# Kernel optimization log

Measured on AMD Instinct MI355X. Metric: run time of the kernel, lower is better.

Reference implementation:

```python
import jax, jax.numpy as jnp
import numpy as np


def setup_inputs() -> dict:
    key = jax.random.key(0)
    ks = jax.random.split(key, 7)
    B, V, D, H = 4, 1024, 3, 128
    vertices = jax.random.normal(ks[0], (B, V, D), dtype=jnp.float32)
    # Linear params (x @ W + b convention, W = torch_weight.T)
    W1 = jax.random.normal(ks[1], (2 * D, H), dtype=jnp.float32) * 0.05
    b1 = jnp.zeros((H,), dtype=jnp.float32)
    W2 = jax.random.normal(ks[2], (H, H // 2), dtype=jnp.float32) * 0.05
    b2 = jnp.zeros((H // 2,), dtype=jnp.float32)
    W3 = jax.random.normal(ks[3], (H // 2, 1), dtype=jnp.float32) * 0.05
    b3 = jnp.zeros((1,), dtype=jnp.float32)
    return {"vertices": vertices, "W1": W1, "b1": b1, "W2": W2, "b2": b2, "W3": W3, "b3": b3}


def reference(vertices, W1, b1, W2, b2, W3, b3):
    B, V, D = vertices.shape
    # All unordered pairs (i, j) with i < j -- same order as the nested loop.
    idx_i, idx_j = jnp.triu_indices(V, k=1)  # each [E], E = V*(V-1)/2
    # Pairwise edge features [B, E, 2D] via gather (no Python loop).
    edge_features = jnp.concatenate(
        [vertices[:, idx_i, :], vertices[:, idx_j, :]], axis=-1
    )
    # 3-layer MLP (dropout is identity in eval mode).
    x = jax.nn.relu(edge_features @ W1 + b1)   # [B, E, H]
    x = jax.nn.relu(x @ W2 + b2)               # [B, E, H//2]
    x = x @ W3 + b3                            # [B, E, 1]
    edge_probs = jax.nn.sigmoid(x[..., 0])     # [B, E]
    edge_indices = jnp.stack([idx_i, idx_j], axis=1)  # [E, 2]
    return edge_probs, edge_indices
```

## Files before the change

### kernel.cpp

```cpp
#include <hip/hip_runtime.h>
#include <hip/hip_bf16.h>
#include <math.h>

#define BB 4
#define VV 1024
#define HH 128
#define H2 64
#define EE 523776
#define BE (BB * EE)
#define TPB (EE / 16)
#define NTILES (BE / 16)
#define NTHR 256
#define NBLK 1024
#define NWAVE (NBLK * 4)

typedef __attribute__((ext_vector_type(8))) short bf16x8;
typedef __attribute__((ext_vector_type(4))) float f32x4;
typedef __attribute__((ext_vector_type(4))) unsigned u32x4;

__device__ __forceinline__ short f2bf(float f) {
    __hip_bfloat16 h = __float2bfloat16(f);
    return *reinterpret_cast<short*>(&h);
}

__device__ __forceinline__ unsigned pkbf(float lo, float hi) {
    return __builtin_amdgcn_perm(__float_as_uint(hi), __float_as_uint(lo),
                                 0x07060302u);
}

__device__ __forceinline__ bf16x8 relu_pack(f32x4 a, f32x4 b) {
    u32x4 r;
    r[0] = pkbf(fmaxf(a[0], 0.f), fmaxf(a[1], 0.f));
    r[1] = pkbf(fmaxf(a[2], 0.f), fmaxf(a[3], 0.f));
    r[2] = pkbf(fmaxf(b[0], 0.f), fmaxf(b[1], 0.f));
    r[3] = pkbf(fmaxf(b[2], 0.f), fmaxf(b[3], 0.f));
    return __builtin_bit_cast(bf16x8, r);
}

__global__ __launch_bounds__(NTHR, 3) void edge_mlp_v11(
    const float* __restrict__ vertices,
    const float* __restrict__ W1,
    const float* __restrict__ b1,
    const float* __restrict__ W2,
    const float* __restrict__ b2,
    const float* __restrict__ W3,
    const float* __restrict__ b3,
    float* __restrict__ out)
{
    __shared__ __align__(16) bf16x8 wA[10 * 64];
    __shared__ __align__(16) f32x4  wC[4 * 64];

    const int lane = threadIdx.x & 63;
    const int col  = lane & 15;
    const int u    = lane >> 4;
    const int wid  = threadIdx.x >> 6;

    const f32x4 zero4 = {0.f, 0.f, 0.f, 0.f};

    bf16x8 A2r[16];
#pragma unroll
    for (int mt = 0; mt < 4; ++mt) {
        const int n2 = 32 * (mt >> 1) + 8 * (col >> 2) + 4 * (mt & 1) + (col & 3);
#pragma unroll
        for (int p = 0; p < 4; ++p)
#pragma unroll
            for (int r = 0; r < 8; ++r)
                A2r[mt * 4 + p][r] = f2bf(W2[(32 * p + 8 * u + r) * H2 + n2]);
    }

    for (int f = wid; f < 14; f += 4) {
        if (f < 8) {
            const int p = f >> 1, q1 = f & 1;
            const int h = 32 * p + 8 * (col >> 2) + 4 * q1 + (col & 3);
            bf16x8 a;
#pragma unroll
            for (int r = 0; r < 8; ++r) {
                const int k = 8 * u + r;
                float w = 0.0f;
                if (k < 6)       w = W1[k * HH + h];
                else if (k == 6) w = b1[h];
                a[r] = f2bf(w);
            }
            wA[f * 64 + lane] = a;
        } else if (f < 10) {
            const int t = f - 8;
            bf16x8 a;
#pragma unroll
            for (int r = 0; r < 8; ++r) a[r] = f2bf(W3[32 * t + 8 * u + r]);
            wA[f * 64 + lane] = a;
        } else {
            const int mt = f - 10;
            f32x4 c;
#pragma unroll
            for (int q = 0; q < 4; ++q)
                c[q] = b2[32 * (mt >> 1) + 8 * u + 4 * (mt & 1) + q];
            wC[mt * 64 + lane] = c;
        }
    }
    const float b3v = b3[0];
    __syncthreads();

    const int gw = blockIdx.x * 4 + wid;

    for (int tt = gw; tt < NTILES; tt += NWAVE) {
        const int b  = tt / TPB;
        const int e0 = (tt - b * TPB) * 16;
        const int e  = e0 + col;

        const int rr = EE - 1 - e;
        const float sq = sqrtf((float)(8 * rr + 1));
        int m = (int)(0.5f * (sq - 1.0f));
        if ((m + 1) * (m + 2) / 2 <= rr) ++m;
        if (m * (m + 1) / 2 > rr) --m;
        const int pp = rr - m * (m + 1) / 2;
        const int iv = VV - 2 - m;
        const int jv = VV - 1 - pp;

        const float* pvi = vertices + (b * VV + iv) * 3;
        const float* pvj = vertices + (b * VV + jv) * 3;
        u32x4 fb;
        fb[0] = pkbf(pvi[0], pvi[1]);
        fb[1] = pkbf(pvi[2], pvj[0]);
        fb[2] = pkbf(pvj[1], pvj[2]);
        fb[3] = 0x00003F80u;
        const bf16x8 bfv = __builtin_bit_cast(bf16x8, fb);

        f32x4 d2_0 = wC[0 * 64 + lane];
        f32x4 d2_1 = wC[1 * 64 + lane];
        f32x4 d2_2 = wC[2 * 64 + lane];
        f32x4 d2_3 = wC[3 * 64 + lane];

#pragma unroll
        for (int p = 0; p < 4; ++p) {
            const bf16x8 a1a = wA[(2 * p + 0) * 64 + lane];
            const bf16x8 a1b = wA[(2 * p + 1) * 64 + lane];
            const f32x4 dA = __builtin_amdgcn_mfma_f32_16x16x32_bf16(a1a, bfv, zero4, 0, 0, 0);
            const f32x4 dB = __builtin_amdgcn_mfma_f32_16x16x32_bf16(a1b, bfv, zero4, 0, 0, 0);
            const bf16x8 Bh = relu_pack(dA, dB);
            d2_0 = __builtin_amdgcn_mfma_f32_16x16x32_bf16(A2r[0 * 4 + p], Bh, d2_0, 0, 0, 0);
            d2_1 = __builtin_amdgcn_mfma_f32_16x16x32_bf16(A2r[1 * 4 + p], Bh, d2_1, 0, 0, 0);
            d2_2 = __builtin_amdgcn_mfma_f32_16x16x32_bf16(A2r[2 * 4 + p], Bh, d2_2, 0, 0, 0);
            d2_3 = __builtin_amdgcn_mfma_f32_16x16x32_bf16(A2r[3 * 4 + p], Bh, d2_3, 0, 0, 0);
        }

        const bf16x8 Bh3_0 = relu_pack(d2_0, d2_1);
        const bf16x8 Bh3_1 = relu_pack(d2_2, d2_3);
        const bf16x8 a30 = wA[8 * 64 + lane];
        const bf16x8 a31 = wA[9 * 64 + lane];
        f32x4 d3 = {b3v, b3v, b3v, b3v};
        d3 = __builtin_amdgcn_mfma_f32_16x16x32_bf16(a30, Bh3_0, d3, 0, 0, 0);
        d3 = __builtin_amdgcn_mfma_f32_16x16x32_bf16(a31, Bh3_1, d3, 0, 0, 0);

        if (u == 0) {
            const float prob = __builtin_amdgcn_rcpf(1.0f + __expf(-d3[0]));
            out[tt * 16 + col] = prob;
            if (b == 0)
                *(float2*)(&out[BE + 2 * e]) = make_float2((float)iv, (float)jv);
        }
    }
}

extern "C" void kernel_launch(void* const* d_in, const int* in_sizes, int n_in,
                              void* d_out, int out_size, void* d_ws, size_t ws_size,
                              hipStream_t stream) {
    const float* vertices = (const float*)d_in[0];
    const float* W1 = (const float*)d_in[1];
    const float* b1 = (const float*)d_in[2];
    const float* W2 = (const float*)d_in[3];
    const float* b2 = (const float*)d_in[4];
    const float* W3 = (const float*)d_in[5];
    const float* b3 = (const float*)d_in[6];
    float* out = (float*)d_out;

    edge_mlp_v11<<<NBLK, NTHR, 0, stream>>>(vertices, W1, b1, W2, b2, W3, b3, out);
}
```

Before: 136.5 us.

## Process four 16-edge subtiles per wave iteration with W2 fragments in LDS

```diff
diff --git a/kernel.cpp b/kernel.cpp
--- a/kernel.cpp
+++ b/kernel.cpp
@@ -8,8 +8,8 @@
 #define H2 64
 #define EE 523776
 #define BE (BB * EE)
-#define TPB (EE / 16)
-#define NTILES (BE / 16)
+#define TPB64 (EE / 64)
+#define NT64 (BE / 64)
 #define NTHR 256
 #define NBLK 1024
 #define NWAVE (NBLK * 4)
@@ -37,7 +37,7 @@
     return __builtin_bit_cast(bf16x8, r);
 }
 
-__global__ __launch_bounds__(NTHR, 3) void edge_mlp_v11(
+__global__ __launch_bounds__(NTHR, 3) void edge_mlp_v12(
     const float* __restrict__ vertices,
     const float* __restrict__ W1,
     const float* __restrict__ b1,
@@ -47,7 +47,7 @@
     const float* __restrict__ b3,
     float* __restrict__ out)
 {
-    __shared__ __align__(16) bf16x8 wA[10 * 64];
+    __shared__ __align__(16) bf16x8 wA[26 * 64];
     __shared__ __align__(16) f32x4  wC[4 * 64];
 
     const int lane = threadIdx.x & 63;
@@ -57,18 +57,7 @@
 
     const f32x4 zero4 = {0.f, 0.f, 0.f, 0.f};
 
-    bf16x8 A2r[16];
-#pragma unroll
-    for (int mt = 0; mt < 4; ++mt) {
-        const int n2 = 32 * (mt >> 1) + 8 * (col >> 2) + 4 * (mt & 1) + (col & 3);
-#pragma unroll
-        for (int p = 0; p < 4; ++p)
-#pragma unroll
-            for (int r = 0; r < 8; ++r)
-                A2r[mt * 4 + p][r] = f2bf(W2[(32 * p + 8 * u + r) * H2 + n2]);
-    }
-
-    for (int f = wid; f < 14; f += 4) {
+    for (int f = wid; f < 30; f += 4) {
         if (f < 8) {
             const int p = f >> 1, q1 = f & 1;
             const int h = 32 * p + 8 * (col >> 2) + 4 * q1 + (col & 3);
@@ -82,14 +71,22 @@
                 a[r] = f2bf(w);
             }
             wA[f * 64 + lane] = a;
-        } else if (f < 10) {
-            const int t = f - 8;
+        } else if (f < 24) {
+            const int mt = (f - 8) >> 2, p = (f - 8) & 3;
+            const int n2 = 32 * (mt >> 1) + 8 * (col >> 2) + 4 * (mt & 1) + (col & 3);
+            bf16x8 a;
+#pragma unroll
+            for (int r = 0; r < 8; ++r)
+                a[r] = f2bf(W2[(32 * p + 8 * u + r) * H2 + n2]);
+            wA[f * 64 + lane] = a;
+        } else if (f < 26) {
+            const int t = f - 24;
             bf16x8 a;
 #pragma unroll
             for (int r = 0; r < 8; ++r) a[r] = f2bf(W3[32 * t + 8 * u + r]);
             wA[f * 64 + lane] = a;
         } else {
-            const int mt = f - 10;
+            const int mt = f - 26;
             f32x4 c;
 #pragma unroll
             for (int q = 0; q < 4; ++q)
@@ -102,60 +99,80 @@
 
     const int gw = blockIdx.x * 4 + wid;
 
-    for (int tt = gw; tt < NTILES; tt += NWAVE) {
-        const int b  = tt / TPB;
-        const int e0 = (tt - b * TPB) * 16;
-        const int e  = e0 + col;
+    for (int tt = gw; tt < NT64; tt += NWAVE) {
+        const int b  = tt / TPB64;
+        const int e0 = (tt - b * TPB64) * 64;
 
-        const int rr = EE - 1 - e;
-        const float sq = sqrtf((float)(8 * rr + 1));
-        int m = (int)(0.5f * (sq - 1.0f));
-        if ((m + 1) * (m + 2) / 2 <= rr) ++m;
-        if (m * (m + 1) / 2 > rr) --m;
-        const int pp = rr - m * (m + 1) / 2;
-        const int iv = VV - 2 - m;
-        const int jv = VV - 1 - pp;
+        bf16x8 bfv[4];
+        int iv[4], jv[4];
+#pragma unroll
+        for (int s = 0; s < 4; ++s) {
+            const int e  = e0 + s * 16 + col;
+            const int rr = EE - 1 - e;
+            const float sq = sqrtf((float)(8 * rr + 1));
+            int m = (int)(0.5f * (sq - 1.0f));
+            if ((m + 1) * (m + 2) / 2 <= rr) ++m;
+            if (m * (m + 1) / 2 > rr) --m;
+            const int pp = rr - m * (m + 1) / 2;
+            iv[s] = VV - 2 - m;
+            jv[s] = VV - 1 - pp;
+            const float* pvi = vertices + (b * VV + iv[s]) * 3;
+            const float* pvj = vertices + (b * VV + jv[s]) * 3;
+            u32x4 fb;
+            fb[0] = pkbf(pvi[0], pvi[1]);
+            fb[1] = pkbf(pvi[2], pvj[0]);
+            fb[2] = pkbf(pvj[1], pvj[2]);
+            fb[3] = 0x00003F80u;
+            bfv[s] = __builtin_bit_cast(bf16x8, fb);
+        }
 
-        const float* pvi = vertices + (b * VV + iv) * 3;
-        const float* pvj = vertices + (b * VV + jv) * 3;
-        u32x4 fb;
-        fb[0] = pkbf(pvi[0], pvi[1]);
-        fb[1] = pkbf(pvi[2], pvj[0]);
-        fb[2] = pkbf(pvj[1], pvj[2]);
-        fb[3] = 0x00003F80u;
-        const bf16x8 bfv = __builtin_bit_cast(bf16x8, fb);
-
-        f32x4 d2_0 = wC[0 * 64 + lane];
-        f32x4 d2_1 = wC[1 * 64 + lane];
-        f32x4 d2_2 = wC[2 * 64 + lane];
-        f32x4 d2_3 = wC[3 * 64 + lane];
+        f32x4 d2[4][4];
+#pragma unroll
+        for (int mt = 0; mt < 4; ++mt) {
+            const f32x4 c = wC[mt * 64 + lane];
+#pragma unroll
+            for (int s = 0; s < 4; ++s) d2[s][mt] = c;
+        }
 
 #pragma unroll
         for (int p = 0; p < 4; ++p) {
             const bf16x8 a1a = wA[(2 * p + 0) * 64 + lane];
             const bf16x8 a1b = wA[(2 * p + 1) * 64 + lane];
-            const f32x4 dA = __builtin_amdgcn_mfma_f32_16x16x32_bf16(a1a, bfv, zero4, 0, 0, 0);
-            const f32x4 dB = __builtin_amdgcn_mfma_f32_16x16x32_bf16(a1b, bfv, zero4, 0, 0, 0);
-            const bf16x8 Bh = relu_pack(dA, dB);
-            d2_0 = __builtin_amdgcn_mfma_f32_16x16x32_bf16(A2r[0 * 4 + p], Bh, d2_0, 0, 0, 0);
-            d2_1 = __builtin_amdgcn_mfma_f32_16x16x32_bf16(A2r[1 * 4 + p], Bh, d2_1, 0, 0, 0);
-            d2_2 = __builtin_amdgcn_mfma_f32_16x16x32_bf16(A2r[2 * 4 + p], Bh, d2_2, 0, 0, 0);
-            d2_3 = __builtin_amdgcn_mfma_f32_16x16x32_bf16(A2r[3 * 4 + p], Bh, d2_3, 0, 0, 0);
+            const bf16x8 w20 = wA[(8 + 0 * 4 + p) * 64 + lane];
+            const bf16x8 w21 = wA[(8 + 1 * 4 + p) * 64 + lane];
+            const bf16x8 w22 = wA[(8 + 2 * 4 + p) * 64 + lane];
+            const bf16x8 w23 = wA[(8 + 3 * 4 + p) * 64 + lane];
+#pragma unroll
+            for (int s = 0; s < 4; ++s) {
+                const f32x4 dA = __builtin_amdgcn_mfma_f32_16x16x32_bf16(a1a, bfv[s], zero4, 0, 0, 0);
+                const f32x4 dB = __builtin_amdgcn_mfma_f32_16x16x32_bf16(a1b, bfv[s], zero4, 0, 0, 0);
+                const bf16x8 Bh = relu_pack(dA, dB);
+                d2[s][0] = __builtin_amdgcn_mfma_f32_16x16x32_bf16(w20, Bh, d2[s][0], 0, 0, 0);
+                d2[s][1] = __builtin_amdgcn_mfma_f32_16x16x32_bf16(w21, Bh, d2[s][1], 0, 0, 0);
+                d2[s][2] = __builtin_amdgcn_mfma_f32_16x16x32_bf16(w22, Bh, d2[s][2], 0, 0, 0);
+                d2[s][3] = __builtin_amdgcn_mfma_f32_16x16x32_bf16(w23, Bh, d2[s][3], 0, 0, 0);
+            }
         }
 
-        const bf16x8 Bh3_0 = relu_pack(d2_0, d2_1);
-        const bf16x8 Bh3_1 = relu_pack(d2_2, d2_3);
-        const bf16x8 a30 = wA[8 * 64 + lane];
-        const bf16x8 a31 = wA[9 * 64 + lane];
-        f32x4 d3 = {b3v, b3v, b3v, b3v};
-        d3 = __builtin_amdgcn_mfma_f32_16x16x32_bf16(a30, Bh3_0, d3, 0, 0, 0);
-        d3 = __builtin_amdgcn_mfma_f32_16x16x32_bf16(a31, Bh3_1, d3, 0, 0, 0);
+        const bf16x8 a30 = wA[24 * 64 + lane];
+        const bf16x8 a31 = wA[25 * 64 + lane];
+#pragma unroll
+        for (int s = 0; s < 4; ++s) {
+            const bf16x8 Bh3_0 = relu_pack(d2[s][0], d2[s][1]);
+            const bf16x8 Bh3_1 = relu_pack(d2[s][2], d2[s][3]);
+            f32x4 d3 = {b3v, b3v, b3v, b3v};
+            d3 = __builtin_amdgcn_mfma_f32_16x16x32_bf16(a30, Bh3_0, d3, 0, 0, 0);
+            d3 = __builtin_amdgcn_mfma_f32_16x16x32_bf16(a31, Bh3_1, d3, 0, 0, 0);
 
-        if (u == 0) {
-            const float prob = __builtin_amdgcn_rcpf(1.0f + __expf(-d3[0]));
-            out[tt * 16 + col] = prob;
-            if (b == 0)
-                *(float2*)(&out[BE + 2 * e]) = make_float2((float)iv, (float)jv);
+            if (u == 0) {
+                const float prob = __builtin_amdgcn_rcpf(1.0f + __expf(-d3[0]));
+                out[tt * 64 + s * 16 + col] = prob;
+                if (b == 0) {
+                    const int e = e0 + s * 16 + col;
+                    *(float2*)(&out[BE + 2 * e]) =
+                        make_float2((float)iv[s], (float)jv[s]);
+                }
+            }
         }
     }
 }
@@ -172,5 +189,5 @@
     const float* b3 = (const float*)d_in[6];
     float* out = (float*)d_out;
 
-    edge_mlp_v11<<<NBLK, NTHR, 0, stream>>>(vertices, W1, b1, W2, b2, W3, b3, out);
+    edge_mlp_v12<<<NBLK, NTHR, 0, stream>>>(vertices, W1, b1, W2, b2, W3, b3, out);
 }
```

Measured after the change: 219.9 us. 61.0% more time.

## Precompute per-vertex layer-1 projections and replace layer-1 MFMAs with gathered adds

Applied to the files above, without the earlier changes.

```diff
diff --git a/kernel.cpp b/kernel.cpp
--- a/kernel.cpp
+++ b/kernel.cpp
@@ -13,6 +13,7 @@
 #define NTHR 256
 #define NBLK 1024
 #define NWAVE (NBLK * 4)
+#define PQN (BB * VV * HH)
 
 typedef __attribute__((ext_vector_type(8))) short bf16x8;
 typedef __attribute__((ext_vector_type(4))) float f32x4;
@@ -37,25 +38,37 @@
     return __builtin_bit_cast(bf16x8, r);
 }
 
-__global__ __launch_bounds__(NTHR, 3) void edge_mlp_v11(
-    const float* __restrict__ vertices,
-    const float* __restrict__ W1,
-    const float* __restrict__ b1,
+__global__ __launch_bounds__(NTHR) void pq_kernel(
+    const float* __restrict__ vertices, const float* __restrict__ W1,
+    const float* __restrict__ b1, float* __restrict__ P, float* __restrict__ Q)
+{
+    const int t = blockIdx.x * NTHR + threadIdx.x;
+    const int v = t >> 7;
+    const int h = t & 127;
+    const float x = vertices[v * 3 + 0];
+    const float y = vertices[v * 3 + 1];
+    const float z = vertices[v * 3 + 2];
+    P[t] = fmaf(x, W1[0 * HH + h], fmaf(y, W1[1 * HH + h], z * W1[2 * HH + h]));
+    Q[t] = fmaf(x, W1[3 * HH + h], fmaf(y, W1[4 * HH + h],
+                fmaf(z, W1[5 * HH + h], b1[h])));
+}
+
+__global__ __launch_bounds__(NTHR, 3) void edge_mlp_v15(
+    const float* __restrict__ P,
+    const float* __restrict__ Q,
     const float* __restrict__ W2,
     const float* __restrict__ b2,
     const float* __restrict__ W3,
     const float* __restrict__ b3,
     float* __restrict__ out)
 {
-    __shared__ __align__(16) bf16x8 wA[10 * 64];
     __shared__ __align__(16) f32x4  wC[4 * 64];
+    __shared__ __align__(16) bf16x8 wA3[2 * 64];
 
     const int lane = threadIdx.x & 63;
     const int col  = lane & 15;
     const int u    = lane >> 4;
     const int wid  = threadIdx.x >> 6;
-
-    const f32x4 zero4 = {0.f, 0.f, 0.f, 0.f};
 
     bf16x8 A2r[16];
 #pragma unroll
@@ -68,39 +81,29 @@
                 A2r[mt * 4 + p][r] = f2bf(W2[(32 * p + 8 * u + r) * H2 + n2]);
     }
 
-    for (int f = wid; f < 14; f += 4) {
-        if (f < 8) {
-            const int p = f >> 1, q1 = f & 1;
-            const int h = 32 * p + 8 * (col >> 2) + 4 * q1 + (col & 3);
-            bf16x8 a;
+    if (wid == 0) {
 #pragma unroll
-            for (int r = 0; r < 8; ++r) {
-                const int k = 8 * u + r;
-                float w = 0.0f;
-                if (k < 6)       w = W1[k * HH + h];
-                else if (k == 6) w = b1[h];
-                a[r] = f2bf(w);
-            }
-            wA[f * 64 + lane] = a;
-        } else if (f < 10) {
-            const int t = f - 8;
-            bf16x8 a;
-#pragma unroll
-            for (int r = 0; r < 8; ++r) a[r] = f2bf(W3[32 * t + 8 * u + r]);
-            wA[f * 64 + lane] = a;
-        } else {
-            const int mt = f - 10;
+        for (int mt = 0; mt < 4; ++mt) {
             f32x4 c;
 #pragma unroll
             for (int q = 0; q < 4; ++q)
                 c[q] = b2[32 * (mt >> 1) + 8 * u + 4 * (mt & 1) + q];
             wC[mt * 64 + lane] = c;
         }
+    } else if (wid == 1) {
+#pragma unroll
+        for (int t = 0; t < 2; ++t) {
+            bf16x8 a;
+#pragma unroll
+            for (int r = 0; r < 8; ++r) a[r] = f2bf(W3[32 * t + 8 * u + r]);
+            wA3[t * 64 + lane] = a;
+        }
     }
     const float b3v = b3[0];
     __syncthreads();
 
     const int gw = blockIdx.x * 4 + wid;
+    const int off0 = 8 * u;
 
     for (int tt = gw; tt < NTILES; tt += NWAVE) {
         const int b  = tt / TPB;
@@ -116,40 +119,41 @@
         const int iv = VV - 2 - m;
         const int jv = VV - 1 - pp;
 
-        const float* pvi = vertices + (b * VV + iv) * 3;
-        const float* pvj = vertices + (b * VV + jv) * 3;
-        u32x4 fb;
-        fb[0] = pkbf(pvi[0], pvi[1]);
-        fb[1] = pkbf(pvi[2], pvj[0]);
-        fb[2] = pkbf(pvj[1], pvj[2]);
-        fb[3] = 0x00003F80u;
-        const bf16x8 bfv = __builtin_bit_cast(bf16x8, fb);
+        const float* Pi = P + (((b << 10) + iv) << 7) + off0;
+        const float* Qj = Q + (((b << 10) + jv) << 7) + off0;
+
+        bf16x8 Bf[4];
+#pragma unroll
+        for (int p = 0; p < 4; ++p) {
+            const float4 pa = *(const float4*)(Pi + 32 * p);
+            const float4 pb = *(const float4*)(Pi + 32 * p + 4);
+            const float4 qa = *(const float4*)(Qj + 32 * p);
+            const float4 qb = *(const float4*)(Qj + 32 * p + 4);
+            u32x4 rrp;
+            rrp[0] = pkbf(fmaxf(pa.x + qa.x, 0.f), fmaxf(pa.y + qa.y, 0.f));
+            rrp[1] = pkbf(fmaxf(pa.z + qa.z, 0.f), fmaxf(pa.w + qa.w, 0.f));
+            rrp[2] = pkbf(fmaxf(pb.x + qb.x, 0.f), fmaxf(pb.y + qb.y, 0.f));
+            rrp[3] = pkbf(fmaxf(pb.z + qb.z, 0.f), fmaxf(pb.w + qb.w, 0.f));
+            Bf[p] = __builtin_bit_cast(bf16x8, rrp);
+        }
 
         f32x4 d2_0 = wC[0 * 64 + lane];
         f32x4 d2_1 = wC[1 * 64 + lane];
         f32x4 d2_2 = wC[2 * 64 + lane];
         f32x4 d2_3 = wC[3 * 64 + lane];
-
 #pragma unroll
         for (int p = 0; p < 4; ++p) {
-            const bf16x8 a1a = wA[(2 * p + 0) * 64 + lane];
-            const bf16x8 a1b = wA[(2 * p + 1) * 64 + lane];
-            const f32x4 dA = __builtin_amdgcn_mfma_f32_16x16x32_bf16(a1a, bfv, zero4, 0, 0, 0);
-            const f32x4 dB = __builtin_amdgcn_mfma_f32_16x16x32_bf16(a1b, bfv, zero4, 0, 0, 0);
-            const bf16x8 Bh = relu_pack(dA, dB);
-            d2_0 = __builtin_amdgcn_mfma_f32_16x16x32_bf16(A2r[0 * 4 + p], Bh, d2_0, 0, 0, 0);
-            d2_1 = __builtin_amdgcn_mfma_f32_16x16x32_bf16(A2r[1 * 4 + p], Bh, d2_1, 0, 0, 0);
-            d2_2 = __builtin_amdgcn_mfma_f32_16x16x32_bf16(A2r[2 * 4 + p], Bh, d2_2, 0, 0, 0);
-            d2_3 = __builtin_amdgcn_mfma_f32_16x16x32_bf16(A2r[3 * 4 + p], Bh, d2_3, 0, 0, 0);
+            d2_0 = __builtin_amdgcn_mfma_f32_16x16x32_bf16(A2r[0 * 4 + p], Bf[p], d2_0, 0, 0, 0);
+            d2_1 = __builtin_amdgcn_mfma_f32_16x16x32_bf16(A2r[1 * 4 + p], Bf[p], d2_1, 0, 0, 0);
+            d2_2 = __builtin_amdgcn_mfma_f32_16x16x32_bf16(A2r[2 * 4 + p], Bf[p], d2_2, 0, 0, 0);
+            d2_3 = __builtin_amdgcn_mfma_f32_16x16x32_bf16(A2r[3 * 4 + p], Bf[p], d2_3, 0, 0, 0);
         }
 
         const bf16x8 Bh3_0 = relu_pack(d2_0, d2_1);
         const bf16x8 Bh3_1 = relu_pack(d2_2, d2_3);
-        const bf16x8 a30 = wA[8 * 64 + lane];
-        const bf16x8 a31 = wA[9 * 64 + lane];
         f32x4 d3 = {b3v, b3v, b3v, b3v};
-        d3 = __builtin_amdgcn_mfma_f32_16x16x32_bf16(a30, Bh3_0, d3, 0, 0, 0);
-        d3 = __builtin_amdgcn_mfma_f32_16x16x32_bf16(a31, Bh3_1, d3, 0, 0, 0);
+        d3 = __builtin_amdgcn_mfma_f32_16x16x32_bf16(wA3[0 * 64 + lane], Bh3_0, d3, 0, 0, 0);
+        d3 = __builtin_amdgcn_mfma_f32_16x16x32_bf16(wA3[1 * 64 + lane], Bh3_1, d3, 0, 0, 0);
 
         if (u == 0) {
             const float prob = __builtin_amdgcn_rcpf(1.0f + __expf(-d3[0]));
@@ -172,5 +176,9 @@
     const float* b3 = (const float*)d_in[6];
     float* out = (float*)d_out;
 
-    edge_mlp_v11<<<NBLK, NTHR, 0, stream>>>(vertices, W1, b1, W2, b2, W3, b3, out);
+    float* P = (float*)d_ws;
+    float* Q = P + PQN;
+
+    pq_kernel<<<PQN / NTHR, NTHR, 0, stream>>>(vertices, W1, b1, P, Q);
+    edge_mlp_v15<<<NBLK, NTHR, 0, stream>>>(P, Q, W2, b2, W3, b3, out);
 }
```

Result: slower. 225.9 us (+65.4%).
